# Kernel optimization log

Measured on AMD Instinct MI355X. Metric: run time of the kernel, lower is better.

The kernel has to match this reference:

```python
import jax, jax.numpy as jnp
import numpy as np

B, S, D, H = 2, 2048, 2048, 16
HD = D // H
WHERE_CONST = -10000.0

def setup_inputs() -> dict:
    key = jax.random.key(0)
    k1, k2, k3 = jax.random.split(key, 3)
    x = jax.random.normal(k1, (B, S, D), dtype=jnp.float32)
    attention_mask = jnp.zeros((B, 1, 1, S), dtype=jnp.float32)
    w_qkv = jax.random.normal(k2, (D, 3 * D), dtype=jnp.float32) * (1.0 / np.sqrt(D))
    b_qkv = jnp.zeros((3 * D,), dtype=jnp.float32)
    w_dense = jax.random.normal(k3, (D, D), dtype=jnp.float32) * (1.0 / np.sqrt(D))
    b_dense = jnp.zeros((D,), dtype=jnp.float32)
    return {"x": x, "attention_mask": attention_mask, "w_qkv": w_qkv,
            "b_qkv": b_qkv, "w_dense": w_dense, "b_dense": b_dense}

def reference(x, attention_mask, w_qkv, b_qkv, w_dense, b_dense):
    # fused QKV projection: [B,S,3D]
    qkv = jnp.einsum('bsd,de->bse', x, w_qkv) + b_qkv
    # [B,S,H,3*hd] -> [B,H,S,3*hd]
    qkv = qkv.reshape(B, S, H, 3 * HD).transpose(0, 2, 1, 3)
    q, k, v = jnp.split(qkv, 3, axis=-1)  # each [B,H,S,hd]
    # scores [B,H,S,S], scaled
    scores = jnp.einsum('bhqd,bhkd->bhqk', q, k) / np.sqrt(HD)
    causal = jnp.tril(jnp.ones((S, S), dtype=bool))[None, None]
    scores = jnp.where(causal, scores, WHERE_CONST)
    scores = scores + attention_mask
    probs = jax.nn.softmax(scores, axis=-1)
    # attention dropout is identity in eval mode
    ctx = jnp.einsum('bhqk,bhkd->bhqd', probs, v)  # [B,H,S,hd]
    ctx = ctx.transpose(0, 2, 1, 3).reshape(B, S, D)
    out = jnp.einsum('bsd,de->bse', ctx, w_dense) + b_dense
    # output dropout is identity in eval mode
    return out
```

## Files before the change

kernel.cpp:

```cpp
#include <hip/hip_runtime.h>
#include <hip/hip_bf16.h>

typedef __bf16 bf16x8 __attribute__((ext_vector_type(8)));
typedef float f32x4 __attribute__((ext_vector_type(4)));
typedef float f32x16 __attribute__((ext_vector_type(16)));
typedef unsigned short u16;

#define S_ 2048
#define D_ 2048
#define H_ 16
#define HD_ 128
#define SCALE_ 0.08838834764831845f

__device__ __forceinline__ u16 f2bf(float f) {
  unsigned u = __builtin_bit_cast(unsigned, f);
  u += 0x7fffu + ((u >> 16) & 1u);
  return (u16)(u >> 16);
}

__device__ __forceinline__ void gload16(void* lds, const void* g) {
  __builtin_amdgcn_global_load_lds((const __attribute__((address_space(1))) void*)g,
                                   (__attribute__((address_space(3))) void*)lds, 16, 0, 0);
}

__device__ __forceinline__ f32x4 mfma16(bf16x8 a, bf16x8 b, f32x4 c) {
  return __builtin_amdgcn_mfma_f32_16x16x32_bf16(a, b, c, 0, 0, 0);
}
__device__ __forceinline__ f32x16 mfma32(bf16x8 a, bf16x8 b, f32x16 c) {
  return __builtin_amdgcn_mfma_f32_32x32x16_bf16(a, b, c, 0, 0, 0);
}

__device__ __forceinline__ unsigned cvt_pk_bf16(float lo, float hi) {
  unsigned r;
  asm("v_cvt_pk_bf16_f32 %0, %1, %2" : "=v"(r) : "v"(lo), "v"(hi));
  return r;
}

__global__ void k_cast_bf16(const float* __restrict__ in, u16* __restrict__ out, int n4) {
  int i = blockIdx.x * blockDim.x + threadIdx.x;
  if (i < n4) {
    float4 v = ((const float4*)in)[i];
    ushort4 o;
    o.x = f2bf(v.x); o.y = f2bf(v.y); o.z = f2bf(v.z); o.w = f2bf(v.w);
    ((ushort4*)out)[i] = o;
  }
}

__global__ void k_transpose_cast(const float* __restrict__ in, u16* __restrict__ out,
                                 int rows, int cols) {
  __shared__ u16 tile[64][66];
  const int c0 = blockIdx.x * 64, r0 = blockIdx.y * 64;
  const int tx = threadIdx.x & 15, ty = threadIdx.x >> 4;
#pragma unroll
  for (int i = 0; i < 4; i++) {
    int r = ty + i * 16;
    float4 v = *(const float4*)&in[(long)(r0 + r) * cols + c0 + tx * 4];
    tile[r][tx * 4 + 0] = f2bf(v.x);
    tile[r][tx * 4 + 1] = f2bf(v.y);
    tile[r][tx * 4 + 2] = f2bf(v.z);
    tile[r][tx * 4 + 3] = f2bf(v.w);
  }
  __syncthreads();
#pragma unroll
  for (int i = 0; i < 4; i++) {
    int cc = ty + i * 16;
    ushort4 o;
    o.x = tile[tx * 4 + 0][cc];
    o.y = tile[tx * 4 + 1][cc];
    o.z = tile[tx * 4 + 2][cc];
    o.w = tile[tx * 4 + 3][cc];
    *(ushort4*)&out[(long)(c0 + cc) * rows + r0 + tx * 4] = o;
  }
}

__device__ __forceinline__ void qkv_store(u16* __restrict__ qb, u16* __restrict__ kpk,
                                          u16* __restrict__ vpk, int row, int col, float val) {
  u16 o = f2bf(val);
  int h = col / 384;
  int m3 = col - h * 384;
  int b = row >> 11, s = row & 2047;
  int bh = b * 16 + h, t = s >> 5;
  if (m3 < 128) {
    qb[(long)row * 2048 + h * 128 + m3] = o;
  } else if (m3 < 256) {
    int dd = m3 - 128;
    long idx = ((((long)bh * 64 + t) * 8 + (dd >> 4)) * 64 + (((dd >> 3) & 1) << 5) + (s & 31)) * 8 + (dd & 7);
    kpk[idx] = o;
  } else {
    int dd = m3 - 256;
    long idx = ((((long)bh * 64 + t) * 8 + (((s >> 4) & 1) << 2) + (dd >> 5)) * 64 + (((s >> 3) & 1) << 5) + (dd & 31)) * 8 + (s & 7);
    vpk[idx] = o;
  }
}

template <int MODE>
__global__ __launch_bounds__(256, 2) void k_gemm(const u16* __restrict__ A,
                                                 const u16* __restrict__ Bt,
                                                 const float* __restrict__ bias,
                                                 void* __restrict__ Cv,
                                                 int M, int N, int K, int NTM,
                                                 u16* __restrict__ qb,
                                                 u16* __restrict__ kpk,
                                                 u16* __restrict__ vpk) {
  __shared__ __align__(16) u16 lA[2][128 * 64];
  __shared__ __align__(16) u16 lB[3][128 * 64];
  const int tid = threadIdx.x, w = tid >> 6, l = tid & 63;
  const int wm = w >> 1, wn = w & 1, lr = l & 15, lg = l >> 4;
  const int nwg = NTM * (N >> 7);
  const int per = nwg >> 3;
  const int tnc = per / NTM;
  const int xcd = (int)blockIdx.x & 7;
  const int local = (int)blockIdx.x >> 3;
  const int ss = local / (8 * tnc), rr = local % (8 * tnc);
  const int tm = (ss * 8 + (rr & 7)) << 7;
  const int tn = (xcd * tnc + (rr >> 3)) << 7;
  const int NT = K >> 6;

  f32x4 acc[4][4];
#pragma unroll
  for (int m = 0; m < 4; m++)
#pragma unroll
    for (int n = 0; n < 4; n++) acc[m][n] = {0.f, 0.f, 0.f, 0.f};

  auto stageA = [&](int buf, int kt) {
#pragma unroll
    for (int i = 0; i < 4; i++) {
      int base = i * 256 + w * 64;
      int f = base + l, r = f >> 3, cg = (f & 7) ^ (r & 7);
      gload16(&lA[buf][base * 8], &A[(long)(tm + r) * K + kt * 64 + cg * 8]);
    }
  };
  auto stageB = [&](int buf, int kt) {
#pragma unroll
    for (int i = 0; i < 4; i++) {
      int base = i * 256 + w * 64;
      int f = base + l, r = f >> 3, cg = (f & 7) ^ (r & 7);
      gload16(&lB[buf][base * 8], &Bt[(long)(tn + r) * K + kt * 64 + cg * 8]);
    }
  };

  stageA(0, 0);
  stageB(0, 0);
  if (NT > 1) { stageA(1, 1); stageB(1, 1); }
  asm volatile("s_waitcnt vmcnt(8)" ::: "memory");
  __builtin_amdgcn_s_barrier();

  for (int kt = 0; kt < NT; ++kt) {
    const int ba = kt & 1;
    const int bb = kt % 3;
    bf16x8 af[4][2], bfr[2][2];
#pragma unroll
    for (int m = 0; m < 4; m++)
#pragma unroll
      for (int k = 0; k < 2; k++) {
        int r = wm * 64 + m * 16 + lr;
        af[m][k] = *(const bf16x8*)&lA[ba][r * 64 + ((((k << 2) + lg) ^ (r & 7)) << 3)];
      }
#pragma unroll
    for (int n = 0; n < 2; n++)
#pragma unroll
      for (int k = 0; k < 2; k++) {
        int r = wn * 64 + n * 16 + lr;
        bfr[n][k] = *(const bf16x8*)&lB[bb][r * 64 + ((((k << 2) + lg) ^ (r & 7)) << 3)];
      }
    if (kt + 2 < NT) stageB((kt + 2) % 3, kt + 2);
    __builtin_amdgcn_s_barrier();
    asm volatile("s_waitcnt lgkmcnt(0)" ::: "memory");
    __builtin_amdgcn_sched_barrier(0);
    __builtin_amdgcn_s_setprio(1);
#pragma unroll
    for (int m = 0; m < 4; m++)
#pragma unroll
      for (int n = 0; n < 2; n++)
#pragma unroll
        for (int k = 0; k < 2; k++)
          acc[m][n] = mfma16(af[m][k], bfr[n][k], acc[m][n]);
    __builtin_amdgcn_s_setprio(0);
    __builtin_amdgcn_s_barrier();

#pragma unroll
    for (int n = 0; n < 2; n++)
#pragma unroll
      for (int k = 0; k < 2; k++) {
        int r = wn * 64 + (n + 2) * 16 + lr;
        bfr[n][k] = *(const bf16x8*)&lB[bb][r * 64 + ((((k << 2) + lg) ^ (r & 7)) << 3)];
      }
    if (kt + 2 < NT) stageA(ba, kt + 2);
    __builtin_amdgcn_s_barrier();
    if (kt + 2 < NT)
      asm volatile("s_waitcnt vmcnt(8) lgkmcnt(0)" ::: "memory");
    else
      asm volatile("s_waitcnt vmcnt(0) lgkmcnt(0)" ::: "memory");
    __builtin_amdgcn_sched_barrier(0);
    __builtin_amdgcn_s_setprio(1);
#pragma unroll
    for (int m = 0; m < 4; m++)
#pragma unroll
      for (int n = 0; n < 2; n++)
#pragma unroll
        for (int k = 0; k < 2; k++)
          acc[m][n + 2] = mfma16(af[m][k], bfr[n][k], acc[m][n + 2]);
    __builtin_amdgcn_s_setprio(0);
    __builtin_amdgcn_s_barrier();
  }

#pragma unroll
  for (int n = 0; n < 4; n++) {
    int col = tn + wn * 64 + n * 16 + lr;
    float bv = bias[col];
#pragma unroll
    for (int m = 0; m < 4; m++) {
      int row0 = tm + wm * 64 + m * 16 + lg * 4;
#pragma unroll
      for (int j = 0; j < 4; j++) {
        float v = acc[m][n][j] + bv;
        if constexpr (MODE == 2)
          qkv_store(qb, kpk, vpk, row0 + j, col, v);
        else
          ((float*)Cv)[(long)(row0 + j) * N + col] = v;
      }
    }
  }
}

__global__ __launch_bounds__(256, 2) void k_attn(const u16* __restrict__ qb,
                                                 const u16* __restrict__ kpk,
                                                 const u16* __restrict__ vpk,
                                                 const float* __restrict__ amask,
                                                 u16* __restrict__ ctx) {
  __shared__ float smO[4][64][65];
  __shared__ float smM[4][32], smL[4][32];
  const int bh = blockIdx.x, b = bh >> 4, h = bh & 15;
  const int tid = threadIdx.x, w = tid >> 6, l = tid & 63;
  const int lr5 = l & 31, hi = l >> 5;
  const int c = 63 - (int)blockIdx.y;
  const int qrow0 = c << 5;
  const int nt = c + 1;

  const u16* kbase = kpk + (long)bh * 64 * 8 * 512 + l * 8;
  const u16* vbase = vpk + (long)bh * 64 * 8 * 512 + l * 8;
  const float* ab0 = amask + b * S_;

  bf16x8 qf[8];
  {
    const u16* qp = qb + (long)(b * S_ + qrow0 + lr5) * 2048 + h * HD_ + hi * 8;
#pragma unroll
    for (int ks = 0; ks < 8; ks++) qf[ks] = *(const bf16x8*)(qp + ks * 16);
  }

  f32x16 aO[4];
#pragma unroll
  for (int db = 0; db < 4; db++)
#pragma unroll
    for (int r = 0; r < 16; r++) aO[db][r] = 0.f;
  float mrun = -3.0e38f, lrun = 0.f;

  const int cnt = (w <= c) ? ((nt - w + 3) >> 2) : 0;

  bf16x8 kA[8], kB[8];
  if (cnt) {
    const u16* kp0 = kbase + (long)w * 4096;
#pragma unroll
    for (int f = 0; f < 8; f++) kA[f] = *(const bf16x8*)(kp0 + f * 512);
  }

  auto body = [&](bf16x8 (&cur)[8], bf16x8 (&nxt)[8], int t, bool pf) {
    const int t32 = t << 5;
    bf16x8 vf[8];
    {
      const u16* vp = vbase + (long)t * 4096;
#pragma unroll
      for (int f = 0; f < 8; f++) vf[f] = *(const bf16x8*)(vp + f * 512);
    }
    f32x4 am[4];
#pragma unroll
    for (int rg = 0; rg < 4; rg++) am[rg] = *(const f32x4*)(ab0 + t32 + rg * 8 + hi * 4);

    f32x16 aS;
#pragma unroll
    for (int r = 0; r < 16; r++) aS[r] = 0.f;
    __builtin_amdgcn_s_setprio(1);
#pragma unroll
    for (int ks = 0; ks < 8; ks++) aS = mfma32(cur[ks], qf[ks], aS);
    __builtin_amdgcn_s_setprio(0);

    if (pf) {
      const u16* kp = kbase + (long)(t + 4) * 4096;
#pragma unroll
      for (int f = 0; f < 8; f++) nxt[f] = *(const bf16x8*)(kp + f * 512);
    }

    float v[16];
    const bool needmask = (t == c);
#pragma unroll
    for (int rg = 0; rg < 4; rg++)
#pragma unroll
      for (int j = 0; j < 4; j++) {
        v[rg * 4 + j] = fmaf(aS[rg * 4 + j], SCALE_, am[rg][j]);
        if (needmask && (rg * 8 + hi * 4 + j > lr5)) v[rg * 4 + j] = -1e30f;
      }
    float mx = v[0];
#pragma unroll
    for (int i = 1; i < 16; i++) mx = fmaxf(mx, v[i]);
    mx = fmaxf(mx, __shfl_xor(mx, 32));

    if (!__all(mx <= mrun + 8.0f)) {
      float mnew = fmaxf(mrun, mx);
      float corr = __expf(mrun - mnew);
      lrun *= corr;
      mrun = mnew;
#pragma unroll
      for (int reg = 0; reg < 16; reg++) {
        float cb = __shfl(corr, (reg & 3) + 8 * (reg >> 2) + 4 * hi);
#pragma unroll
        for (int db = 0; db < 4; db++) aO[db][reg] *= cb;
      }
    }

    float ls = 0.f;
#pragma unroll
    for (int i = 0; i < 16; i++) { v[i] = __expf(v[i] - mrun); ls += v[i]; }
    ls += __shfl_xor(ls, 32);
    lrun += ls;

    unsigned pk[8];
#pragma unroll
    for (int q = 0; q < 8; q++) pk[q] = cvt_pk_bf16(v[2 * q], v[2 * q + 1]);
    bf16x8 pa[2];
#pragma unroll
    for (int kst = 0; kst < 2; kst++) {
      unsigned a0 = pk[4 * kst], a1 = pk[4 * kst + 1], a2 = pk[4 * kst + 2], a3 = pk[4 * kst + 3];
      unsigned s0 = hi ? a0 : a2;
      unsigned s1 = hi ? a1 : a3;
      unsigned r0 = __shfl_xor(s0, 32);
      unsigned r1 = __shfl_xor(s1, 32);
      union { unsigned u[4]; bf16x8 vv; } U;
      U.u[0] = hi ? r0 : a0;
      U.u[1] = hi ? r1 : a1;
      U.u[2] = hi ? a2 : r0;
      U.u[3] = hi ? a3 : r1;
      pa[kst] = U.vv;
    }

    __builtin_amdgcn_s_setprio(1);
#pragma unroll
    for (int kst = 0; kst < 2; kst++)
#pragma unroll
      for (int db = 0; db < 4; db++)
        aO[db] = mfma32(pa[kst], vf[kst * 4 + db], aO[db]);
    __builtin_amdgcn_s_setprio(0);
  };

  for (int i = 0; i < cnt; i += 2) {
    body(kA, kB, w + 4 * i, i + 1 < cnt);
    if (i + 1 < cnt) body(kB, kA, w + 4 * (i + 1), i + 2 < cnt);
  }

#pragma unroll
  for (int db = 0; db < 4; db++)
#pragma unroll
    for (int reg = 0; reg < 16; reg++) smO[w][l][db * 16 + reg] = aO[db][reg];
  if (hi == 0) { smM[w][lr5] = mrun; smL[w][lr5] = lrun; }
  __syncthreads();

  {
    const int db = w;
#pragma unroll
    for (int reg = 0; reg < 16; reg++) {
      int r = (reg & 3) + 8 * (reg >> 2) + 4 * hi;
      float m0 = smM[0][r], m1 = smM[1][r], m2 = smM[2][r], m3 = smM[3][r];
      float ms = fmaxf(fmaxf(m0, m1), fmaxf(m2, m3));
      float f0 = __expf(m0 - ms), f1 = __expf(m1 - ms);
      float f2 = __expf(m2 - ms), f3 = __expf(m3 - ms);
      float lsum = smL[0][r] * f0 + smL[1][r] * f1 + smL[2][r] * f2 + smL[3][r] * f3;
      float val = smO[0][l][db * 16 + reg] * f0 + smO[1][l][db * 16 + reg] * f1 +
                  smO[2][l][db * 16 + reg] * f2 + smO[3][l][db * 16 + reg] * f3;
      int srow = qrow0 + r;
      ctx[(long)(b * S_ + srow) * D_ + h * HD_ + db * 32 + lr5] = f2bf(val / lsum);
    }
  }
}

extern "C" void kernel_launch(void* const* d_in, const int* in_sizes, int n_in,
                              void* d_out, int out_size, void* d_ws, size_t ws_size,
                              hipStream_t stream) {
  const float* x  = (const float*)d_in[0];
  const float* am = (const float*)d_in[1];
  const float* wq = (const float*)d_in[2];
  const float* bq = (const float*)d_in[3];
  const float* wd = (const float*)d_in[4];
  const float* bd = (const float*)d_in[5];
  float* out = (float*)d_out;
  char* ws = (char*)d_ws;

  const size_t MB = 1048576;
  u16* xb   = (u16*)(ws);
  u16* wqT  = (u16*)(ws + 16 * MB);
  u16* qb   = (u16*)(ws + 40 * MB);
  u16* kpk  = (u16*)(ws + 56 * MB);
  u16* vpk  = (u16*)(ws + 72 * MB);
  u16* ctxb = (u16*)(ws);
  u16* wdT  = (u16*)(ws + 16 * MB);

  k_cast_bf16<<<8192, 256, 0, stream>>>(x, xb, 2097152);
  k_transpose_cast<<<dim3(96, 32), 256, 0, stream>>>(wq, wqT, 2048, 6144);
  k_gemm<2><<<1536, 256, 0, stream>>>(xb, wqT, bq, nullptr, 4096, 6144, 2048, 32, qb, kpk, vpk);
  k_transpose_cast<<<dim3(32, 32), 256, 0, stream>>>(wd, wdT, 2048, 2048);
  k_attn<<<dim3(32, 64), 256, 0, stream>>>(qb, kpk, vpk, am, ctxb);
  k_gemm<0><<<512, 256, 0, stream>>>(ctxb, wdT, bd, out, 4096, 2048, 2048, 32,
                                     nullptr, nullptr, nullptr);
}
```

Baseline: 256.0 us.

## Widen GEMM tile to 128x256 with 8 waves and four-phase pipeline

Replaces the 256-thread 128x128 GEMM with a 512-thread kernel computing 128x256 output tiles, splitting each k-step into four MFMA quadrants interleaved with half-tile B loads and a next-step A load. Larger tiles raise arithmetic intensity and reduce global traffic per FLOP, and the finer phase split aims to overlap loads with compute. LDS grows to about 128KB per block, which drops occupancy to one block per CU, and the wait-count logic is more intricate.

```diff
diff --git a/kernel.cpp b/kernel.cpp
--- a/kernel.cpp
+++ b/kernel.cpp
@@ -94,26 +94,26 @@
 }
 
 template <int MODE>
-__global__ __launch_bounds__(256, 2) void k_gemm(const u16* __restrict__ A,
-                                                 const u16* __restrict__ Bt,
-                                                 const float* __restrict__ bias,
-                                                 void* __restrict__ Cv,
-                                                 int M, int N, int K, int NTM,
-                                                 u16* __restrict__ qb,
-                                                 u16* __restrict__ kpk,
-                                                 u16* __restrict__ vpk) {
+__global__ __launch_bounds__(512) void k_gemm8(const u16* __restrict__ A,
+                                               const u16* __restrict__ Bt,
+                                               const float* __restrict__ bias,
+                                               void* __restrict__ Cv,
+                                               int M, int N, int K, int NTM,
+                                               u16* __restrict__ qb,
+                                               u16* __restrict__ kpk,
+                                               u16* __restrict__ vpk) {
   __shared__ __align__(16) u16 lA[2][128 * 64];
-  __shared__ __align__(16) u16 lB[3][128 * 64];
+  __shared__ __align__(16) u16 lB[3][256 * 64];
   const int tid = threadIdx.x, w = tid >> 6, l = tid & 63;
-  const int wm = w >> 1, wn = w & 1, lr = l & 15, lg = l >> 4;
-  const int nwg = NTM * (N >> 7);
+  const int wm = w >> 2, wn = w & 3, lr = l & 15, lg = l >> 4;
+  const int nwg = NTM * (N >> 8);
   const int per = nwg >> 3;
   const int tnc = per / NTM;
   const int xcd = (int)blockIdx.x & 7;
   const int local = (int)blockIdx.x >> 3;
   const int ss = local / (8 * tnc), rr = local % (8 * tnc);
   const int tm = (ss * 8 + (rr & 7)) << 7;
-  const int tn = (xcd * tnc + (rr >> 3)) << 7;
+  const int tn = (xcd * tnc + (rr >> 3)) << 8;
   const int NT = K >> 6;
 
   f32x4 acc[4][4];
@@ -124,57 +124,61 @@
 
   auto stageA = [&](int buf, int kt) {
 #pragma unroll
-    for (int i = 0; i < 4; i++) {
-      int base = i * 256 + w * 64;
+    for (int i = 0; i < 2; i++) {
+      int base = i * 512 + w * 64;
       int f = base + l, r = f >> 3, cg = (f & 7) ^ (r & 7);
       gload16(&lA[buf][base * 8], &A[(long)(tm + r) * K + kt * 64 + cg * 8]);
     }
   };
-  auto stageB = [&](int buf, int kt) {
-#pragma unroll
-    for (int i = 0; i < 4; i++) {
-      int base = i * 256 + w * 64;
+  auto stageBh = [&](int buf, int kt, int hf) {
+#pragma unroll
+    for (int i = 0; i < 2; i++) {
+      int base = i * 512 + w * 64;
       int f = base + l, r = f >> 3, cg = (f & 7) ^ (r & 7);
-      gload16(&lB[buf][base * 8], &Bt[(long)(tn + r) * K + kt * 64 + cg * 8]);
+      gload16(&lB[buf][(hf * 1024 + base) * 8],
+              &Bt[(long)(tn + hf * 128 + r) * K + kt * 64 + cg * 8]);
     }
   };
 
   stageA(0, 0);
-  stageB(0, 0);
-  if (NT > 1) { stageA(1, 1); stageB(1, 1); }
-  asm volatile("s_waitcnt vmcnt(8)" ::: "memory");
+  stageBh(0, 0, 0); stageBh(0, 0, 1);
+  if (NT > 1) { stageBh(1, 1, 0); stageBh(1, 1, 1); }
+  asm volatile("s_waitcnt vmcnt(4)" ::: "memory");
   __builtin_amdgcn_s_barrier();
 
   for (int kt = 0; kt < NT; ++kt) {
     const int ba = kt & 1;
     const int bb = kt % 3;
-    bf16x8 af[4][2], bfr[2][2];
-#pragma unroll
-    for (int m = 0; m < 4; m++)
+    bf16x8 aL[2][2], aH[2][2], b01[2][2], b23[2][2];
+    const int rowA = wm * 64;
+    const int rowB = wn * 64;
+
+#pragma unroll
+    for (int m = 0; m < 2; m++)
 #pragma unroll
       for (int k = 0; k < 2; k++) {
-        int r = wm * 64 + m * 16 + lr;
-        af[m][k] = *(const bf16x8*)&lA[ba][r * 64 + ((((k << 2) + lg) ^ (r & 7)) << 3)];
+        int r = rowA + m * 16 + lr;
+        aL[m][k] = *(const bf16x8*)&lA[ba][r * 64 + ((((k << 2) + lg) ^ (r & 7)) << 3)];
       }
 #pragma unroll
     for (int n = 0; n < 2; n++)
 #pragma unroll
       for (int k = 0; k < 2; k++) {
-        int r = wn * 64 + n * 16 + lr;
-        bfr[n][k] = *(const bf16x8*)&lB[bb][r * 64 + ((((k << 2) + lg) ^ (r & 7)) << 3)];
-      }
-    if (kt + 2 < NT) stageB((kt + 2) % 3, kt + 2);
+        int r = rowB + n * 16 + lr;
+        b01[n][k] = *(const bf16x8*)&lB[bb][r * 64 + ((((k << 2) + lg) ^ (r & 7)) << 3)];
+      }
+    if (kt + 1 < NT) stageA(ba ^ 1, kt + 1);
     __builtin_amdgcn_s_barrier();
     asm volatile("s_waitcnt lgkmcnt(0)" ::: "memory");
     __builtin_amdgcn_sched_barrier(0);
     __builtin_amdgcn_s_setprio(1);
 #pragma unroll
-    for (int m = 0; m < 4; m++)
+    for (int m = 0; m < 2; m++)
 #pragma unroll
       for (int n = 0; n < 2; n++)
 #pragma unroll
         for (int k = 0; k < 2; k++)
-          acc[m][n] = mfma16(af[m][k], bfr[n][k], acc[m][n]);
+          acc[m][n] = mfma16(aL[m][k], b01[n][k], acc[m][n]);
     __builtin_amdgcn_s_setprio(0);
     __builtin_amdgcn_s_barrier();
 
@@ -182,24 +186,60 @@
     for (int n = 0; n < 2; n++)
 #pragma unroll
       for (int k = 0; k < 2; k++) {
-        int r = wn * 64 + (n + 2) * 16 + lr;
-        bfr[n][k] = *(const bf16x8*)&lB[bb][r * 64 + ((((k << 2) + lg) ^ (r & 7)) << 3)];
-      }
-    if (kt + 2 < NT) stageA(ba, kt + 2);
+        int r = rowB + (n + 2) * 16 + lr;
+        b23[n][k] = *(const bf16x8*)&lB[bb][r * 64 + ((((k << 2) + lg) ^ (r & 7)) << 3)];
+      }
+    if (kt + 2 < NT) stageBh((kt + 2) % 3, kt + 2, 0);
+    __builtin_amdgcn_s_barrier();
+    asm volatile("s_waitcnt lgkmcnt(0)" ::: "memory");
+    __builtin_amdgcn_sched_barrier(0);
+    __builtin_amdgcn_s_setprio(1);
+#pragma unroll
+    for (int m = 0; m < 2; m++)
+#pragma unroll
+      for (int n = 0; n < 2; n++)
+#pragma unroll
+        for (int k = 0; k < 2; k++)
+          acc[m][n + 2] = mfma16(aL[m][k], b23[n][k], acc[m][n + 2]);
+    __builtin_amdgcn_s_setprio(0);
+    __builtin_amdgcn_s_barrier();
+
+#pragma unroll
+    for (int m = 0; m < 2; m++)
+#pragma unroll
+      for (int k = 0; k < 2; k++) {
+        int r = rowA + (m + 2) * 16 + lr;
+        aH[m][k] = *(const bf16x8*)&lA[ba][r * 64 + ((((k << 2) + lg) ^ (r & 7)) << 3)];
+      }
+    if (kt + 2 < NT) stageBh((kt + 2) % 3, kt + 2, 1);
+    __builtin_amdgcn_s_barrier();
+    asm volatile("s_waitcnt lgkmcnt(0)" ::: "memory");
+    __builtin_amdgcn_sched_barrier(0);
+    __builtin_amdgcn_s_setprio(1);
+#pragma unroll
+    for (int m = 0; m < 2; m++)
+#pragma unroll
+      for (int n = 0; n < 2; n++)
+#pragma unroll
+        for (int k = 0; k < 2; k++)
+          acc[m + 2][n] = mfma16(aH[m][k], b01[n][k], acc[m + 2][n]);
+    __builtin_amdgcn_s_setprio(0);
+    __builtin_amdgcn_s_barrier();
+
     __builtin_amdgcn_s_barrier();
     if (kt + 2 < NT)
-      asm volatile("s_waitcnt vmcnt(8) lgkmcnt(0)" ::: "memory");
+      asm volatile("s_waitcnt vmcnt(4)" ::: "memory");
     else
-      asm volatile("s_waitcnt vmcnt(0) lgkmcnt(0)" ::: "memory");
+      asm volatile("s_waitcnt vmcnt(0)" ::: "memory");
     __builtin_amdgcn_sched_barrier(0);
     __builtin_amdgcn_s_setprio(1);
 #pragma unroll
-    for (int m = 0; m < 4; m++)
+    for (int m = 0; m < 2; m++)
 #pragma unroll
       for (int n = 0; n < 2; n++)
 #pragma unroll
         for (int k = 0; k < 2; k++)
-          acc[m][n + 2] = mfma16(af[m][k], bfr[n][k], acc[m][n + 2]);
+          acc[m + 2][n + 2] = mfma16(aH[m][k], b23[n][k], acc[m + 2][n + 2]);
     __builtin_amdgcn_s_setprio(0);
     __builtin_amdgcn_s_barrier();
   }
@@ -404,9 +444,9 @@
 
   k_cast_bf16<<<8192, 256, 0, stream>>>(x, xb, 2097152);
   k_transpose_cast<<<dim3(96, 32), 256, 0, stream>>>(wq, wqT, 2048, 6144);
-  k_gemm<2><<<1536, 256, 0, stream>>>(xb, wqT, bq, nullptr, 4096, 6144, 2048, 32, qb, kpk, vpk);
+  k_gemm8<2><<<768, 512, 0, stream>>>(xb, wqT, bq, nullptr, 4096, 6144, 2048, 32, qb, kpk, vpk);
   k_transpose_cast<<<dim3(32, 32), 256, 0, stream>>>(wd, wdT, 2048, 2048);
   k_attn<<<dim3(32, 64), 256, 0, stream>>>(qb, kpk, vpk, am, ctxb);
-  k_gemm<0><<<512, 256, 0, stream>>>(ctxb, wdT, bd, out, 4096, 2048, 2048, 32,
-                                     nullptr, nullptr, nullptr);
-}
+  k_gemm8<0><<<256, 512, 0, stream>>>(ctxb, wdT, bd, out, 4096, 2048, 2048, 32,
+                                      nullptr, nullptr, nullptr);
+}
```

Measured after the change: 285.2 us. 11.4% more time.
